# Kernel optimization log

Hardware: AMD Instinct MI355X
Metric: run time of the kernel (lower is better)

The kernel has to match this reference:

```python
import jax, jax.numpy as jnp
import numpy as np

EPS = 1e-05


def layer_norm(x, scale):
    # Faithful to source bug: returns scale * x_norm + scale (shift param unused)
    mean = jnp.mean(x, axis=-1, keepdims=True)
    var = jnp.var(x, axis=-1, keepdims=True)  # unbiased=False
    x_norm = (x - mean) / jnp.sqrt(var + EPS)
    return scale * x_norm + scale


def mhsa(x, wq, wk, wv, wo, bo, n_heads):
    b, t, d = x.shape
    hd = d // n_heads
    # torch Linear: y = x @ W.T (no qkv bias)
    q = (x @ wq.T).reshape(b, t, n_heads, hd).transpose(0, 2, 1, 3)  # bhtd
    k = (x @ wk.T).reshape(b, t, n_heads, hd).transpose(0, 2, 1, 3)
    v = (x @ wv.T).reshape(b, t, n_heads, hd).transpose(0, 2, 1, 3)
    scores = jnp.einsum('bhqd,bhkd->bhqk', q, k)
    causal = jnp.triu(jnp.ones((t, t), dtype=bool), k=1)
    scores = jnp.where(causal, -jnp.inf, scores)
    attn = jax.nn.softmax(scores / np.sqrt(hd).astype(np.float32), axis=-1)
    ctx = jnp.einsum('bhqk,bhkd->bhqd', attn, v)
    ctx = ctx.transpose(0, 2, 1, 3).reshape(b, t, d)
    return ctx @ wo.T + bo


def setup_inputs() -> dict:
    key = jax.random.key(0)
    ks = jax.random.split(key, 6)
    B, T, D = 2, 2048, 1024
    return {
        'x': jax.random.normal(ks[0], (B, T, D), dtype=jnp.float32),
        'wq': jax.random.normal(ks[1], (D, D), dtype=jnp.float32) * 0.02,
        'wk': jax.random.normal(ks[2], (D, D), dtype=jnp.float32) * 0.02,
        'wv': jax.random.normal(ks[3], (D, D), dtype=jnp.float32) * 0.02,
        'wo': jax.random.normal(ks[4], (D, D), dtype=jnp.float32) * 0.02,
        'bo': jnp.zeros((D,), dtype=jnp.float32),
        'ln1_scale': jnp.ones((D,), dtype=jnp.float32),
        'ln2_scale': jnp.ones((D,), dtype=jnp.float32),
    }


def reference(x, wq, wk, wv, wo, bo, ln1_scale, ln2_scale):
    n_heads = 16
    # Block 1: norm1 -> attn -> (+residual); dropout is identity in eval mode
    h = x + mhsa(layer_norm(x, ln1_scale), wq, wk, wv, wo, bo, n_heads)
    # Block 2: source calls self.attn (same weights) again, not self.ff
    out = h + mhsa(layer_norm(h, ln2_scale), wq, wk, wv, wo, bo, n_heads)
    return out
```

## Files before the change

kernel.cpp:

```cpp
#include <hip/hip_runtime.h>
#include <hip/hip_bf16.h>
#include <math.h>

#define Dm 1024
#define Tm 2048
#define Bm 2
#define Hm 16
#define HDm 64
#define Rm (Bm*Tm)
#define QKS 2048

typedef __attribute__((ext_vector_type(8))) short sh8;
typedef __attribute__((ext_vector_type(4))) float f32x4;

#define AS1(p) ((const __attribute__((address_space(1))) void*)(p))
#define AS3(p) ((__attribute__((address_space(3))) void*)(p))

__device__ __forceinline__ short f2bs(float f) {
    union { float f; unsigned u; } v; v.f = f;
    unsigned r = v.u + 0x7FFFu + ((v.u >> 16) & 1u);
    return (short)(r >> 16);
}

__global__ __launch_bounds__(256) void convert_w(const float* __restrict__ wq,
                                                 const float* __restrict__ wk,
                                                 const float* __restrict__ wv,
                                                 const float* __restrict__ wo,
                                                 short* __restrict__ wqkv,
                                                 short* __restrict__ wob) {
    int idx = (blockIdx.x * 256 + threadIdx.x) * 4;
    const int M1 = 1 << 20;
    const float* src; short* dst; int off;
    if (idx < M1)           { src = wq; dst = wqkv;          off = idx; }
    else if (idx < 2*M1)    { src = wk; dst = wqkv + M1;     off = idx - M1; }
    else if (idx < 3*M1)    { src = wv; dst = wqkv + 2*M1;   off = idx - 2*M1; }
    else                    { src = wo; dst = wob;           off = idx - 3*M1; }
    float4 v = *(const float4*)(src + off);
    short4 o;
    o.x = f2bs(v.x); o.y = f2bs(v.y); o.z = f2bs(v.z); o.w = f2bs(v.w);
    *(short4*)(dst + off) = o;
}

__global__ __launch_bounds__(256) void ln_kernel(const float* __restrict__ x,
                                                 const float* __restrict__ scale,
                                                 short* __restrict__ out) {
    int row = blockIdx.x;
    int t = threadIdx.x;
    const float4* xr = (const float4*)(x + (size_t)row * Dm);
    float4 v = xr[t];
    float s  = v.x + v.y + v.z + v.w;
    float ss = v.x*v.x + v.y*v.y + v.z*v.z + v.w*v.w;
    #pragma unroll
    for (int off = 32; off; off >>= 1) {
        s  += __shfl_xor(s, off);
        ss += __shfl_xor(ss, off);
    }
    __shared__ float red[8];
    int wave = t >> 6, lane = t & 63;
    if (lane == 0) { red[wave*2] = s; red[wave*2+1] = ss; }
    __syncthreads();
    s  = red[0] + red[2] + red[4] + red[6];
    ss = red[1] + red[3] + red[5] + red[7];
    float mean = s * (1.0f / Dm);
    float var  = ss * (1.0f / Dm) - mean * mean;
    float rstd = 1.0f / sqrtf(var + 1e-5f);
    float4 sc = ((const float4*)scale)[t];
    short4 o;
    o.x = f2bs(sc.x * ((v.x - mean) * rstd) + sc.x);
    o.y = f2bs(sc.y * ((v.y - mean) * rstd) + sc.y);
    o.z = f2bs(sc.z * ((v.z - mean) * rstd) + sc.z);
    o.w = f2bs(sc.w * ((v.w - mean) * rstd) + sc.w);
    ((short4*)(out + (size_t)row * Dm))[t] = o;
}

template<int BN, int MODE>
__global__ __launch_bounds__(256) void gemm_mfma(const short* __restrict__ A,
                                                 const short* __restrict__ B,
                                                 const float* __restrict__ bias,
                                                 const float* __restrict__ res,
                                                 void* __restrict__ Cv,
                                                 short* __restrict__ Vt,
                                                 int M, int N, int K) {
    __shared__ short As[128*32];
    __shared__ short Bs[BN*32];
    __shared__ short Tb[(MODE==1) ? 4*16*68 : 4];
    const int NJ = BN / 32;
    int t = threadIdx.x;
    int lane = t & 63, w = t >> 6;
    int l = lane & 15, quad = lane >> 4;
    int wm = (w & 1) * 64, wn = (w >> 1) * (BN/2);
    int m0 = blockIdx.y * 128, n0 = blockIdx.x * BN;

    f32x4 acc[4][NJ];
    #pragma unroll
    for (int i = 0; i < 4; i++)
        #pragma unroll
        for (int j = 0; j < NJ; j++)
            acc[i][j] = (f32x4){0.f,0.f,0.f,0.f};

    for (int k0 = 0; k0 < K; k0 += 32) {
        __syncthreads();
        #pragma unroll
        for (int p = 0; p < 2; p++) {
            int off = p*4096 + t*16;
            int row = off >> 6;
            int c = ((off >> 4) & 3) ^ (row & 3);
            const short* ga = A + (size_t)(m0 + row) * K + k0 + c*8;
            __builtin_amdgcn_global_load_lds(AS1(ga), AS3((char*)As + off), 16, 0, 0);
        }
        #pragma unroll
        for (int p = 0; p < BN/64; p++) {
            int off = p*4096 + t*16;
            int row = off >> 6;
            int c = ((off >> 4) & 3) ^ (row & 3);
            const short* gb = B + (size_t)(n0 + row) * K + k0 + c*8;
            __builtin_amdgcn_global_load_lds(AS1(gb), AS3((char*)Bs + off), 16, 0, 0);
        }
        __syncthreads();
        sh8 af[4], bf[NJ];
        #pragma unroll
        for (int i = 0; i < 4; i++) {
            int m = wm + i*16 + l;
            af[i] = *(const sh8*)((const char*)As + m*64 + ((quad ^ (m & 3)) * 16));
        }
        #pragma unroll
        for (int j = 0; j < NJ; j++) {
            int n = wn + j*16 + l;
            bf[j] = *(const sh8*)((const char*)Bs + n*64 + ((quad ^ (n & 3)) * 16));
        }
        #pragma unroll
        for (int i = 0; i < 4; i++)
            #pragma unroll
            for (int j = 0; j < NJ; j++)
                acc[i][j] = __builtin_amdgcn_mfma_f32_16x16x32_bf16(af[i], bf[j], acc[i][j], 0, 0, 0);
    }
    if (MODE == 0) {
        #pragma unroll
        for (int i = 0; i < 4; i++)
            #pragma unroll
            for (int j = 0; j < NJ; j++)
                #pragma unroll
                for (int r = 0; r < 4; r++) {
                    int m = m0 + wm + i*16 + quad*4 + r;
                    int n = n0 + wn + j*16 + l;
                    float vv = acc[i][j][r] + bias[n] + res[(size_t)m * N + n];
                    ((float*)Cv)[(size_t)m * N + n] = vv;
                }
    } else {
        if (n0 < 2048) {
            #pragma unroll
            for (int i = 0; i < 4; i++)
                #pragma unroll
                for (int j = 0; j < NJ; j++)
                    #pragma unroll
                    for (int r = 0; r < 4; r++) {
                        int m = m0 + wm + i*16 + quad*4 + r;
                        int n = n0 + wn + j*16 + l;
                        ((short*)Cv)[(size_t)m * QKS + n] = f2bs(acc[i][j][r]);
                    }
        } else {
            int bq = m0 >> 11;
            int key0 = (m0 & 2047) + wm;
            int h = (n0 + wn - 2048) >> 6;
            short* vout = Vt + ((size_t)(bq*Hm + h) * HDm) * Tm + key0;
            #pragma unroll
            for (int j = 0; j < NJ; j++) {
                #pragma unroll
                for (int i = 0; i < 4; i++) {
                    short4 o;
                    o.x = f2bs(acc[i][j][0]); o.y = f2bs(acc[i][j][1]);
                    o.z = f2bs(acc[i][j][2]); o.w = f2bs(acc[i][j][3]);
                    *(short4*)&Tb[w*(16*68) + l*68 + i*16 + quad*4] = o;
                }
                #pragma unroll
                for (int st = 0; st < 2; st++) {
                    int rr = st*8 + (lane >> 3);
                    int cc = lane & 7;
                    sh8 vv = *(const sh8*)&Tb[w*(16*68) + rr*68 + cc*8];
                    *(sh8*)(vout + (size_t)(j*16 + rr) * Tm + cc*8) = vv;
                }
            }
        }
    }
}

__device__ __forceinline__ void stage_kv(const short* kp0, const short* vh,
                                         int kbase, short* Kd, short* Vd, int t) {
    #pragma unroll
    for (int p = 0; p < 2; p++) {
        int off = p*4096 + t*16;
        int row = off >> 7;
        int c = ((off >> 4) & 7) ^ (row & 7);
        const short* gk = kp0 + (size_t)(kbase + row) * QKS + c*8;
        __builtin_amdgcn_global_load_lds(AS1(gk), AS3((char*)Kd + off), 16, 0, 0);
        const short* gv = vh + (size_t)row * Tm + kbase + c*8;
        __builtin_amdgcn_global_load_lds(AS1(gv), AS3((char*)Vd + off), 16, 0, 0);
    }
}

__global__ __launch_bounds__(256) void attn_mfma(const short* __restrict__ qk,
                                                 const short* __restrict__ vtg,
                                                 short* __restrict__ ctx) {
    __shared__ short Kl[2][64*64];
    __shared__ short Vl[2][64*64];
    __shared__ short Pl[4][16*64];
    int t = threadIdx.x;
    int lane = t & 63, w = t >> 6;
    int l = lane & 15, quad = lane >> 4;
    int bh = blockIdx.x;
    int xi = blockIdx.y;
    int cc0 = xi & 7, kk0 = xi >> 3;
    int qt = (kk0 == 0) ? cc0 : (kk0 == 1) ? (15 - cc0)
           : (kk0 == 2) ? (16 + cc0) : (31 - cc0);
    int b = bh >> 4, h = bh & 15;
    size_t rbase = (size_t)b * Tm;
    const short* qp0 = qk + rbase * QKS + h*HDm;
    const short* kp0 = qp0 + Dm;
    const short* vh  = vtg + ((size_t)bh * HDm) * Tm;
    int qtbase = qt * 64;

    sh8 qf0, qf1;
    {
        const short* qp = qp0 + (size_t)(qtbase + w*16 + l) * QKS + quad*8;
        qf0 = *(const sh8*)qp;
        qf1 = *(const sh8*)(qp + 32);
    }
    f32x4 O[4] = {{0,0,0,0},{0,0,0,0},{0,0,0,0},{0,0,0,0}};
    float ps[4] = {0.f, 0.f, 0.f, 0.f};

    int cur = 0;
    stage_kv(kp0, vh, 0, Kl[0], Vl[0], t);
    __syncthreads();

    int swl = l & 7;
    for (int kc = 0; kc <= qt; kc++) {
        int kbase = kc * 64;
        if (kc < qt)
            stage_kv(kp0, vh, kbase + 64, Kl[cur^1], Vl[cur^1], t);

        f32x4 S[4];
        #pragma unroll
        for (int kt = 0; kt < 4; kt++) {
            const f32x4 z = {0.f,0.f,0.f,0.f};
            int key = kt*16 + l;
            const char* kb = (const char*)Kl[cur] + key*128;
            int sw = key & 7;
            sh8 k0 = *(const sh8*)(kb + ((quad ^ sw) * 16));
            sh8 k1 = *(const sh8*)(kb + (((4 + quad) ^ sw) * 16));
            f32x4 s = __builtin_amdgcn_mfma_f32_16x16x32_bf16(k0, qf0, z, 0, 0, 0);
            s = __builtin_amdgcn_mfma_f32_16x16x32_bf16(k1, qf1, s, 0, 0, 0);
            S[kt] = s;
        }
        bool needmask = (kbase + 63 > qtbase + w*16);
        int qrow = qtbase + w*16 + l;
        #pragma unroll
        for (int kt = 0; kt < 4; kt++) {
            float p[4];
            if (needmask) {
                #pragma unroll
                for (int r = 0; r < 4; r++) {
                    int key = kbase + kt*16 + quad*4 + r;
                    p[r] = (key > qrow) ? 0.f : __expf(S[kt][r] * 0.125f);
                }
            } else {
                #pragma unroll
                for (int r = 0; r < 4; r++)
                    p[r] = __expf(S[kt][r] * 0.125f);
            }
            ps[kt] += (p[0] + p[1]) + (p[2] + p[3]);
            __hip_bfloat162 pa = __float22bfloat162_rn({p[0], p[1]});
            __hip_bfloat162 pb = __float22bfloat162_rn({p[2], p[3]});
            union { __hip_bfloat162 hh[2]; short4 s4; } u;
            u.hh[0] = pa; u.hh[1] = pb;
            int g = (kt*2 + (quad >> 1)) ^ swl;
            *(short4*)&Pl[w][l*64 + g*8 + (quad & 1)*4] = u.s4;
        }
        sh8 p0 = *(const sh8*)&Pl[w][l*64 + ((quad ^ swl) * 8)];
        sh8 p1 = *(const sh8*)&Pl[w][l*64 + (((4 + quad) ^ swl) * 8)];
        #pragma unroll
        for (int dt = 0; dt < 4; dt++) {
            int d = dt*16 + l;
            const char* vb = (const char*)Vl[cur] + d*128;
            int sw = d & 7;
            sh8 v0 = *(const sh8*)(vb + ((quad ^ sw) * 16));
            sh8 v1 = *(const sh8*)(vb + (((4 + quad) ^ sw) * 16));
            O[dt] = __builtin_amdgcn_mfma_f32_16x16x32_bf16(p0, v0, O[dt], 0, 0, 0);
            O[dt] = __builtin_amdgcn_mfma_f32_16x16x32_bf16(p1, v1, O[dt], 0, 0, 0);
        }
        __syncthreads();
        cur ^= 1;
    }

    float psum = (ps[0] + ps[1]) + (ps[2] + ps[3]);
    psum += __shfl_xor(psum, 16);
    psum += __shfl_xor(psum, 32);
    #pragma unroll
    for (int r = 0; r < 4; r++) {
        int src = (lane & 48) | (((lane >> 4) << 2) + r);
        float inv = 1.0f / __shfl(psum, src);
        int row = qtbase + w*16 + quad*4 + r;
        #pragma unroll
        for (int dt = 0; dt < 4; dt++)
            ctx[(rbase + row) * Dm + h*HDm + dt*16 + l] = f2bs(O[dt][r] * inv);
    }
}

extern "C" void kernel_launch(void* const* d_in, const int* in_sizes, int n_in,
                              void* d_out, int out_size, void* d_ws, size_t ws_size,
                              hipStream_t stream) {
    const float* x   = (const float*)d_in[0];
    const float* wq  = (const float*)d_in[1];
    const float* wk  = (const float*)d_in[2];
    const float* wv  = (const float*)d_in[3];
    const float* wo  = (const float*)d_in[4];
    const float* bo  = (const float*)d_in[5];
    const float* ln1 = (const float*)d_in[6];
    const float* ln2 = (const float*)d_in[7];
    float* out = (float*)d_out;

    short* lnb  = (short*)d_ws;
    short* ctxb = lnb  + (size_t)Rm*Dm;
    short* qk   = ctxb + (size_t)Rm*Dm;
    short* vtg  = qk   + (size_t)Rm*QKS;
    short* wqkv = vtg  + (size_t)Bm*Hm*HDm*Tm;
    short* wob  = wqkv + (size_t)3*Dm*Dm;

    dim3 qgrid(3072/128, Rm/128);
    dim3 pgrid(Dm/64,    Rm/128);
    dim3 agrid(32, 32);

    convert_w<<<4096, 256, 0, stream>>>(wq, wk, wv, wo, wqkv, wob);

    ln_kernel<<<Rm, 256, 0, stream>>>(x, ln1, lnb);
    gemm_mfma<128, 1><<<qgrid, 256, 0, stream>>>(lnb, wqkv, nullptr, nullptr, qk, vtg, Rm, 3072, Dm);
    attn_mfma<<<agrid, 256, 0, stream>>>(qk, vtg, ctxb);
    gemm_mfma<64, 0><<<pgrid, 256, 0, stream>>>(ctxb, wob, bo, x, out, nullptr, Rm, Dm, Dm);

    ln_kernel<<<Rm, 256, 0, stream>>>(out, ln2, lnb);
    gemm_mfma<128, 1><<<qgrid, 256, 0, stream>>>(lnb, wqkv, nullptr, nullptr, qk, vtg, Rm, 3072, Dm);
    attn_mfma<<<agrid, 256, 0, stream>>>(qk, vtg, ctxb);
    gemm_mfma<64, 0><<<pgrid, 256, 0, stream>>>(ctxb, wob, bo, out, out, nullptr, Rm, Dm, Dm);
}
```

Baseline: 303.8 us.

## Fold softmax scale into Wq, hoist KV staging pointers, add MFMA priority, widen proj tile

The 1/sqrt(hd) factor is multiplied into Wq during bf16 conversion, which removes a per-score multiply in the attention loop. K/V staging addresses are now computed once and advanced by pointer increments instead of being recomputed each iteration. s_setprio raises wave priority around the MFMA sections. The output projection GEMM switches from a 64-wide to a 128-wide N tile, which halves its grid to 256 blocks and may lower occupancy. Scaling Wq before rounding to bf16 changes rounding slightly, though scaling by a power of two is exact.

```diff
diff --git a/kernel.cpp b/kernel.cpp
--- a/kernel.cpp
+++ b/kernel.cpp
@@ -30,14 +30,14 @@
                                                  short* __restrict__ wob) {
     int idx = (blockIdx.x * 256 + threadIdx.x) * 4;
     const int M1 = 1 << 20;
-    const float* src; short* dst; int off;
-    if (idx < M1)           { src = wq; dst = wqkv;          off = idx; }
+    const float* src; short* dst; int off; float sc = 1.0f;
+    if (idx < M1)           { src = wq; dst = wqkv;          off = idx; sc = 0.125f; }
     else if (idx < 2*M1)    { src = wk; dst = wqkv + M1;     off = idx - M1; }
     else if (idx < 3*M1)    { src = wv; dst = wqkv + 2*M1;   off = idx - 2*M1; }
     else                    { src = wo; dst = wob;           off = idx - 3*M1; }
     float4 v = *(const float4*)(src + off);
     short4 o;
-    o.x = f2bs(v.x); o.y = f2bs(v.y); o.z = f2bs(v.z); o.w = f2bs(v.w);
+    o.x = f2bs(v.x*sc); o.y = f2bs(v.y*sc); o.z = f2bs(v.z*sc); o.w = f2bs(v.w*sc);
     *(short4*)(dst + off) = o;
 }
 
@@ -181,20 +181,6 @@
                 }
             }
         }
-    }
-}
-
-__device__ __forceinline__ void stage_kv(const short* kp0, const short* vh,
-                                         int kbase, short* Kd, short* Vd, int t) {
-    #pragma unroll
-    for (int p = 0; p < 2; p++) {
-        int off = p*4096 + t*16;
-        int row = off >> 7;
-        int c = ((off >> 4) & 7) ^ (row & 7);
-        const short* gk = kp0 + (size_t)(kbase + row) * QKS + c*8;
-        __builtin_amdgcn_global_load_lds(AS1(gk), AS3((char*)Kd + off), 16, 0, 0);
-        const short* gv = vh + (size_t)row * Tm + kbase + c*8;
-        __builtin_amdgcn_global_load_lds(AS1(gv), AS3((char*)Vd + off), 16, 0, 0);
     }
 }
 
@@ -228,17 +214,35 @@
     f32x4 O[4] = {{0,0,0,0},{0,0,0,0},{0,0,0,0},{0,0,0,0}};
     float ps[4] = {0.f, 0.f, 0.f, 0.f};
 
+    int offA = t*16, offB = 4096 + t*16;
+    int rowA = offA >> 7, rowB = offB >> 7;
+    int swA = ((offA >> 4) & 7) ^ (rowA & 7);
+    int swB = ((offB >> 4) & 7) ^ (rowB & 7);
+    const short* gkA = kp0 + (size_t)rowA * QKS + swA*8;
+    const short* gkB = kp0 + (size_t)rowB * QKS + swB*8;
+    const short* gvA = vh + (size_t)rowA * Tm + swA*8;
+    const short* gvB = vh + (size_t)rowB * Tm + swB*8;
+
+#define STAGE(KD, VD) do { \
+    __builtin_amdgcn_global_load_lds(AS1(gkA), AS3((char*)(KD) + offA), 16, 0, 0); \
+    __builtin_amdgcn_global_load_lds(AS1(gkB), AS3((char*)(KD) + offB), 16, 0, 0); \
+    __builtin_amdgcn_global_load_lds(AS1(gvA), AS3((char*)(VD) + offA), 16, 0, 0); \
+    __builtin_amdgcn_global_load_lds(AS1(gvB), AS3((char*)(VD) + offB), 16, 0, 0); \
+    gkA += 64*QKS; gkB += 64*QKS; gvA += 64; gvB += 64; } while (0)
+
+    STAGE(Kl[0], Vl[0]);
+    __syncthreads();
+
+    int swl = l & 7;
     int cur = 0;
-    stage_kv(kp0, vh, 0, Kl[0], Vl[0], t);
-    __syncthreads();
-
-    int swl = l & 7;
     for (int kc = 0; kc <= qt; kc++) {
         int kbase = kc * 64;
-        if (kc < qt)
-            stage_kv(kp0, vh, kbase + 64, Kl[cur^1], Vl[cur^1], t);
+        if (kc < qt) {
+            if (cur) STAGE(Kl[0], Vl[0]); else STAGE(Kl[1], Vl[1]);
+        }
 
         f32x4 S[4];
+        __builtin_amdgcn_s_setprio(1);
         #pragma unroll
         for (int kt = 0; kt < 4; kt++) {
             const f32x4 z = {0.f,0.f,0.f,0.f};
@@ -251,6 +255,7 @@
             s = __builtin_amdgcn_mfma_f32_16x16x32_bf16(k1, qf1, s, 0, 0, 0);
             S[kt] = s;
         }
+        __builtin_amdgcn_s_setprio(0);
         bool needmask = (kbase + 63 > qtbase + w*16);
         int qrow = qtbase + w*16 + l;
         #pragma unroll
@@ -260,12 +265,12 @@
                 #pragma unroll
                 for (int r = 0; r < 4; r++) {
                     int key = kbase + kt*16 + quad*4 + r;
-                    p[r] = (key > qrow) ? 0.f : __expf(S[kt][r] * 0.125f);
+                    p[r] = (key > qrow) ? 0.f : __expf(S[kt][r]);
                 }
             } else {
                 #pragma unroll
                 for (int r = 0; r < 4; r++)
-                    p[r] = __expf(S[kt][r] * 0.125f);
+                    p[r] = __expf(S[kt][r]);
             }
             ps[kt] += (p[0] + p[1]) + (p[2] + p[3]);
             __hip_bfloat162 pa = __float22bfloat162_rn({p[0], p[1]});
@@ -277,6 +282,7 @@
         }
         sh8 p0 = *(const sh8*)&Pl[w][l*64 + ((quad ^ swl) * 8)];
         sh8 p1 = *(const sh8*)&Pl[w][l*64 + (((4 + quad) ^ swl) * 8)];
+        __builtin_amdgcn_s_setprio(1);
         #pragma unroll
         for (int dt = 0; dt < 4; dt++) {
             int d = dt*16 + l;
@@ -287,9 +293,11 @@
             O[dt] = __builtin_amdgcn_mfma_f32_16x16x32_bf16(p0, v0, O[dt], 0, 0, 0);
             O[dt] = __builtin_amdgcn_mfma_f32_16x16x32_bf16(p1, v1, O[dt], 0, 0, 0);
         }
+        __builtin_amdgcn_s_setprio(0);
         __syncthreads();
         cur ^= 1;
     }
+#undef STAGE
 
     float psum = (ps[0] + ps[1]) + (ps[2] + ps[3]);
     psum += __shfl_xor(psum, 16);
@@ -326,7 +334,7 @@
     short* wob  = wqkv + (size_t)3*Dm*Dm;
 
     dim3 qgrid(3072/128, Rm/128);
-    dim3 pgrid(Dm/64,    Rm/128);
+    dim3 pgrid(Dm/128,   Rm/128);
     dim3 agrid(32, 32);
 
     convert_w<<<4096, 256, 0, stream>>>(wq, wk, wv, wo, wqkv, wob);
@@ -334,10 +342,10 @@
     ln_kernel<<<Rm, 256, 0, stream>>>(x, ln1, lnb);
     gemm_mfma<128, 1><<<qgrid, 256, 0, stream>>>(lnb, wqkv, nullptr, nullptr, qk, vtg, Rm, 3072, Dm);
     attn_mfma<<<agrid, 256, 0, stream>>>(qk, vtg, ctxb);
-    gemm_mfma<64, 0><<<pgrid, 256, 0, stream>>>(ctxb, wob, bo, x, out, nullptr, Rm, Dm, Dm);
+    gemm_mfma<128, 0><<<pgrid, 256, 0, stream>>>(ctxb, wob, bo, x, out, nullptr, Rm, Dm, Dm);
 
     ln_kernel<<<Rm, 256, 0, stream>>>(out, ln2, lnb);
     gemm_mfma<128, 1><<<qgrid, 256, 0, stream>>>(lnb, wqkv, nullptr, nullptr, qk, vtg, Rm, 3072, Dm);
     attn_mfma<<<agrid, 256, 0, stream>>>(qk, vtg, ctxb);
-    gemm_mfma<64, 0><<<pgrid, 256, 0, stream>>>(ctxb, wob, bo, out, out, nullptr, Rm, Dm, Dm);
-}
+    gemm_mfma<128, 0><<<pgrid, 256, 0, stream>>>(ctxb, wob, bo, out, out, nullptr, Rm, Dm, Dm);
+}
```

After: 312.1 us. 2.7% more time.
